# Kernel tuning notes

Hardware: AMD Instinct MI355X
Metric: run time of the kernel (lower is better)

## Reference

```python
import jax, jax.numpy as jnp
import numpy as np
from jax import lax

NUM_HEADS = 8
HEAD_DIM = 32
DIM = NUM_HEADS * HEAD_DIM  # 256
SR = 2
B, H, W = 4, 64, 64


def setup_inputs() -> dict:
    key = jax.random.key(0)
    ks = jax.random.split(key, 6)
    x = jax.random.normal(ks[0], (B, DIM, H, W), dtype=jnp.float32)
    # query: 1x1 conv without bias -> plain [out,in] matrix
    Wq = jax.random.normal(ks[1], (DIM, DIM), dtype=jnp.float32) * (1.0 / np.sqrt(DIM))
    # key/value: sr x sr conv, stride sr, no bias (OIHW)
    Wk = jax.random.normal(ks[2], (DIM, DIM, SR, SR), dtype=jnp.float32) * (1.0 / np.sqrt(DIM * SR * SR))
    Wv = jax.random.normal(ks[3], (DIM, DIM, SR, SR), dtype=jnp.float32) * (1.0 / np.sqrt(DIM * SR * SR))
    rel_h = jax.random.normal(ks[4], (1, NUM_HEADS, HEAD_DIM, 1, H // SR), dtype=jnp.float32)
    rel_w = jax.random.normal(ks[5], (1, NUM_HEADS, HEAD_DIM, W // SR, 1), dtype=jnp.float32)
    return {"x": x, "Wq": Wq, "Wk": Wk, "Wv": Wv, "rel_h": rel_h, "rel_w": rel_w}


def reference(x, Wq, Wk, Wv, rel_h, rel_w):
    b, c, h, w = x.shape
    nh, hd = NUM_HEADS, HEAD_DIM
    scale = hd ** (-0.5)
    dn = ('NCHW', 'OIHW', 'NCHW')

    # q: 1x1 conv == channel matmul; [B, C, H*W] -> [B, nh, hd, Nq]
    q = jnp.einsum('oc,bchw->bohw', Wq, x).reshape(b, nh, hd, h * w)
    # k, v: sr x sr conv, stride sr -> [B, nh, hd, Nkv]
    k = lax.conv_general_dilated(x, Wk, window_strides=(SR, SR), padding='VALID',
                                 dimension_numbers=dn).reshape(b, nh, hd, -1)
    v = lax.conv_general_dilated(x, Wv, window_strides=(SR, SR), padding='VALID',
                                 dimension_numbers=dn).reshape(b, nh, hd, -1)

    # attn scores: q^T k -> [B, nh, Nq, Nkv]
    attn = jnp.einsum('bhdn,bhdm->bhnm', q, k)
    # relative positional bias: (rel_h + rel_w) broadcast -> [nh, hd, Nkv]
    pos = (rel_h + rel_w).reshape(nh, hd, -1)
    attn = attn + jnp.einsum('bhdn,hdm->bhnm', q, pos)
    attn = jax.nn.softmax(attn * scale, axis=-1)

    # out = v @ attn^T -> [B, nh, hd, Nq] -> [B, C, H, W]
    out = jnp.einsum('bhdm,bhnm->bhdn', v, attn).reshape(b, c, h, w)
    return out
```

## Files before the change

kernel.cpp:

```cpp
#include <hip/hip_runtime.h>
#include <math.h>


typedef __bf16 bf16;
typedef __attribute__((ext_vector_type(4))) __bf16 bf16x4;
typedef __attribute__((ext_vector_type(8))) __bf16 bf16x8;
typedef __attribute__((ext_vector_type(4))) float f32x4;
typedef __attribute__((ext_vector_type(2))) __fp16 fp16x2_raw;
typedef __attribute__((ext_vector_type(4))) _Float16 f16x4;

#define MFMA16 __builtin_amdgcn_mfma_f32_16x16x32_bf16
#define MFMA16H __builtin_amdgcn_mfma_f32_16x16x16f16

#define QSCALE 0.25503486f
#define SOFTMAX_SHIFT 10.0f

__global__ void k_prep_w(const float* __restrict__ Wq, const float* __restrict__ Wk,
                         const float* __restrict__ Wv,
                         bf16* __restrict__ Wq_bf, bf16* __restrict__ Wkv_bf) {
    int tid = blockIdx.x * 256 + threadIdx.x;
    int c = tid >> 8, i = tid & 255;
    const float* Wsrc = (c < 256) ? Wk : Wv;
    int cs = c & 255;
    f32x4 w4 = ((const f32x4*)Wsrc)[cs * 256 + i];
#pragma unroll
    for (int tap = 0; tap < 4; tap++)
        Wkv_bf[c * 1024 + tap * 256 + i] = (bf16)w4[tap];
    if (tid < 16384) {
        f32x4 q4 = ((const f32x4*)Wq)[tid];
        bf16x4 o;
#pragma unroll
        for (int e = 0; e < 4; e++) o[e] = (bf16)(q4[e] * QSCALE);
        *(bf16x4*)(Wq_bf + tid * 4) = o;
    }
}

__global__ void k_xT(const float* __restrict__ x, bf16* __restrict__ xT) {
    int b = blockIdx.z, c0 = blockIdx.y * 64, n0 = blockIdx.x * 64;
    __shared__ float tile[64][65];
    int t = threadIdx.x;
    const float* xp = x + (size_t)(b * 256 + c0) * 4096 + n0;
#pragma unroll
    for (int k2 = 0; k2 < 16; k2++) {
        int flat = k2 * 256 + t;
        int row = flat >> 6, col = flat & 63;
        tile[row][col] = xp[(size_t)row * 4096 + col];
    }
    __syncthreads();
    bf16* op = xT + (size_t)(b * 4096 + n0) * 256 + c0;
#pragma unroll
    for (int k2 = 0; k2 < 16; k2++) {
        int flat = k2 * 256 + t;
        int row = flat >> 6, col = flat & 63;
        op[(size_t)row * 256 + col] = (bf16)tile[col][row];
    }
}

__launch_bounds__(256)
__global__ void k_gemm_kv(const bf16* __restrict__ xT, const bf16* __restrict__ Wkv_bf,
                          const float* __restrict__ rel_h, const float* __restrict__ rel_w,
                          bf16* __restrict__ kpos_t, _Float16* __restrict__ v_td) {
    int b = blockIdx.z;
    int bx = blockIdx.x;
    int m0 = bx * 32;
    int c0w = blockIdx.y * 64 + (threadIdx.x >> 6) * 16;
    int t = threadIdx.x, l = t & 63;
    int lr = l & 15, lg = l >> 4;
    __shared__ __align__(16) bf16 Ps[2][32 * 264];
    const bf16* xb = xT + (size_t)b * 4096 * 256;
    int srow = t >> 3;
    int scu0 = (t & 7) * 4;
    uint4 pre[4];
#define LOAD_CHUNK(tap)                                                        \
    {                                                                          \
        int dy = (tap) >> 1, dx = (tap) & 1;                                   \
        const bf16* src = xb + (size_t)((2 * bx + dy) * 64 + 2 * srow + dx) * 256; \
        _Pragma("unroll")                                                      \
        for (int j = 0; j < 4; j++)                                            \
            pre[j] = *(const uint4*)(src + (scu0 + j) * 8);                    \
    }
#define WRITE_CHUNK(buf)                                                       \
    {                                                                          \
        bf16* dst = Ps[buf] + srow * 264 + scu0 * 8;                           \
        _Pragma("unroll")                                                      \
        for (int j = 0; j < 4; j++) *(uint4*)(dst + j * 8) = pre[j];           \
    }
    LOAD_CHUNK(0)
    WRITE_CHUNK(0)
    const bf16* Gkb = Wkv_bf + (size_t)(c0w + lr) * 1024 + lg * 8;
    const bf16* Gvb = Gkb + 256 * 1024;
    f32x4 accK[2] = {}, accV[2] = {};
    for (int ch = 0; ch < 4; ch++) {
        if (ch < 3) LOAD_CHUNK(ch + 1)
        __syncthreads();
        const bf16* P = Ps[ch & 1];
#pragma unroll
        for (int kk = 0; kk < 8; kk++) {
            bf16x8 pa0 = *(const bf16x8*)(P + lr * 264 + kk * 32 + lg * 8);
            bf16x8 pa1 = *(const bf16x8*)(P + (16 + lr) * 264 + kk * 32 + lg * 8);
            bf16x8 gk = *(const bf16x8*)(Gkb + ch * 256 + kk * 32);
            bf16x8 gv = *(const bf16x8*)(Gvb + ch * 256 + kk * 32);
            accK[0] = MFMA16(pa0, gk, accK[0], 0, 0, 0);
            accK[1] = MFMA16(pa1, gk, accK[1], 0, 0, 0);
            accV[0] = MFMA16(gv, pa0, accV[0], 0, 0, 0);
            accV[1] = MFMA16(gv, pa1, accV[1], 0, 0, 0);
        }
        if (ch < 3) {
            __syncthreads();
            WRITE_CHUNK((ch + 1) & 1)
        }
    }
    {
        int cc = c0w + lr;
        float rw = rel_w[cc * 32 + bx];
#pragma unroll
        for (int i = 0; i < 2; i++)
#pragma unroll
            for (int r = 0; r < 4; r++) {
                int ml = i * 16 + lg * 4 + r;
                float val = accK[i][r] + rw + rel_h[cc * 32 + ml];
                kpos_t[((size_t)(b * 8 + (cc >> 5)) * 1024 + m0 + ml) * 32 + (cc & 31)] = (bf16)val;
            }
    }
#pragma unroll
    for (int j = 0; j < 2; j++) {
        int m = m0 + j * 16 + lr;
#pragma unroll
        for (int r = 0; r < 4; r++) {
            int cc = c0w + lg * 4 + r;
            v_td[((size_t)(b * 8 + (cc >> 5)) * 32 + (cc & 31)) * 1024 + m] = (_Float16)accV[j][r];
        }
    }
#undef LOAD_CHUNK
#undef WRITE_CHUNK
}

__launch_bounds__(256)
__global__ void k_attn(const bf16* __restrict__ xT, const bf16* __restrict__ Wq_bf,
                       const bf16* __restrict__ kpos_t, const _Float16* __restrict__ v_td,
                       float* __restrict__ out) {
    int b = blockIdx.z, h = blockIdx.y;
    int t = threadIdx.x;
    int w = t >> 6, l = t & 63;
    int n0 = blockIdx.x * 128 + w * 32;
    int lr = l & 15, lg = l >> 4;
    const size_t bh = (size_t)(b * 8 + h);
    __shared__ __align__(16) bf16 Ks[2][128 * 32];
    __shared__ __align__(16) _Float16 Vs[2][32][136];
    const bf16* Kb = kpos_t + bh * 1024 * 32;
    const _Float16* Vb = v_td + bh * 32 * 1024;
    bf16* Qs = (bf16*)Ks + w * 1280;
    {
        const bf16* Aw = Wq_bf + (size_t)(h * 32 + lr) * 256 + lg * 8;
        const bf16* Bx = xT + (size_t)(b * 4096 + n0 + lr) * 256 + lg * 8;
        f32x4 aq[2][2] = {};
#pragma unroll
        for (int kk = 0; kk < 8; kk++) {
            bf16x8 a0 = *(const bf16x8*)(Aw + kk * 32);
            bf16x8 a1 = *(const bf16x8*)(Aw + 16 * 256 + kk * 32);
            bf16x8 b0 = *(const bf16x8*)(Bx + kk * 32);
            bf16x8 b1 = *(const bf16x8*)(Bx + 16 * 256 + kk * 32);
            aq[0][0] = MFMA16(a0, b0, aq[0][0], 0, 0, 0);
            aq[0][1] = MFMA16(a0, b1, aq[0][1], 0, 0, 0);
            aq[1][0] = MFMA16(a1, b0, aq[1][0], 0, 0, 0);
            aq[1][1] = MFMA16(a1, b1, aq[1][1], 0, 0, 0);
        }
#pragma unroll
        for (int i = 0; i < 2; i++)
#pragma unroll
            for (int j = 0; j < 2; j++) {
                bf16x4 pk;
#pragma unroll
                for (int r = 0; r < 4; r++) pk[r] = (bf16)aq[i][j][r];
                *(bf16x4*)(Qs + (j * 16 + lr) * 40 + i * 16 + lg * 4) = pk;
            }
    }
    bf16x8 bq0, bq1;
    {
        bf16x4 a0 = *(const bf16x4*)(Qs + lr * 40 + lg * 8);
        bf16x4 a1 = *(const bf16x4*)(Qs + lr * 40 + lg * 8 + 4);
        bf16x4 b0 = *(const bf16x4*)(Qs + (16 + lr) * 40 + lg * 8);
        bf16x4 b1 = *(const bf16x4*)(Qs + (16 + lr) * 40 + lg * 8 + 4);
#pragma unroll
        for (int e = 0; e < 4; e++) {
            bq0[e] = a0[e]; bq0[4 + e] = a1[e];
            bq1[e] = b0[e]; bq1[4 + e] = b1[e];
        }
    }
    __syncthreads();
#define STAGE(ch, buf)                                                         \
    {                                                                          \
        const uint4* ksrc = (const uint4*)(Kb + (size_t)(ch) * 128 * 32);      \
        _Pragma("unroll")                                                      \
        for (int j = 0; j < 2; j++) {                                          \
            int u = t + j * 256;                        \
            int m = u >> 2;                                                    \
            int phys = ((m >> 1) + (u & 3)) & 3;                               \
            *(uint4*)(&Ks[buf][m * 32 + phys * 8]) = ksrc[u];                  \
        }                                                                      \
        _Pragma("unroll")                                                      \
        for (int j = 0; j < 2; j++) {                                          \
            int u = t + j * 256;                        \
            *(uint4*)(&Vs[buf][u >> 4][(u & 15) * 8]) =                        \
                *(const uint4*)(Vb + (size_t)(u >> 4) * 1024 + (ch) * 128 +    \
                                (u & 15) * 8);                                 \
        }                                                                      \
    }
    STAGE(0, 0)
    f32x4 accO[2][2] = {};
    f32x4 accS0 = {}, accS1 = {};
    const f16x4 onesv = {(_Float16)1.f, (_Float16)1.f, (_Float16)1.f, (_Float16)1.f};
    const f32x4 zs = {-SOFTMAX_SHIFT, -SOFTMAX_SHIFT, -SOFTMAX_SHIFT, -SOFTMAX_SHIFT};
    const int koff = (((lr >> 1) + lg) & 3) * 8;
    for (int ch = 0; ch < 8; ch++) {
        __syncthreads();
        if (ch < 7) STAGE(ch + 1, (ch + 1) & 1)
        const bf16* Kc = Ks[ch & 1];
#pragma unroll
        for (int tt = 0; tt < 8; tt++) {
            bf16x8 ak = *(const bf16x8*)(Kc + (tt * 16 + lr) * 32 + koff);
            f32x4 s0 = MFMA16(ak, bq0, zs, 0, 0, 0);
            f32x4 s1 = MFMA16(ak, bq1, zs, 0, 0, 0);
            f16x4 p0, p1;
            {
                fp16x2_raw c01 = __builtin_amdgcn_cvt_pkrtz(
                    __builtin_amdgcn_exp2f(s0[0]), __builtin_amdgcn_exp2f(s0[1]));
                fp16x2_raw c23 = __builtin_amdgcn_cvt_pkrtz(
                    __builtin_amdgcn_exp2f(s0[2]), __builtin_amdgcn_exp2f(s0[3]));
                p0[0] = c01[0]; p0[1] = c01[1]; p0[2] = c23[0]; p0[3] = c23[1];
                fp16x2_raw d01 = __builtin_amdgcn_cvt_pkrtz(
                    __builtin_amdgcn_exp2f(s1[0]), __builtin_amdgcn_exp2f(s1[1]));
                fp16x2_raw d23 = __builtin_amdgcn_cvt_pkrtz(
                    __builtin_amdgcn_exp2f(s1[2]), __builtin_amdgcn_exp2f(s1[3]));
                p1[0] = d01[0]; p1[1] = d01[1]; p1[2] = d23[0]; p1[3] = d23[1];
            }
            f16x4 v0 = *(const f16x4*)(&Vs[ch & 1][lr][tt * 16 + lg * 4]);
            f16x4 v1 = *(const f16x4*)(&Vs[ch & 1][16 + lr][tt * 16 + lg * 4]);
            accO[0][0] = MFMA16H(p0, v0, accO[0][0], 0, 0, 0);
            accO[0][1] = MFMA16H(p0, v1, accO[0][1], 0, 0, 0);
            accS0      = MFMA16H(p0, onesv, accS0, 0, 0, 0);
            accO[1][0] = MFMA16H(p1, v0, accO[1][0], 0, 0, 0);
            accO[1][1] = MFMA16H(p1, v1, accO[1][1], 0, 0, 0);
            accS1      = MFMA16H(p1, onesv, accS1, 0, 0, 0);
        }
    }
#undef STAGE
    float inv0[4], inv1[4];
#pragma unroll
    for (int r = 0; r < 4; r++) {
        inv0[r] = 1.0f / accS0[r];
        inv1[r] = 1.0f / accS1[r];
    }
#pragma unroll
    for (int dt = 0; dt < 2; dt++) {
        int c = h * 32 + dt * 16 + lr;
        float* op0 = out + (size_t)(b * 256 + c) * 4096 + n0 + lg * 4;
        float* op1 = op0 + 16;
        f32x4 o0, o1;
#pragma unroll
        for (int r = 0; r < 4; r++) {
            o0[r] = accO[0][dt][r] * inv0[r];
            o1[r] = accO[1][dt][r] * inv1[r];
        }
        *(f32x4*)op0 = o0;
        *(f32x4*)op1 = o1;
    }
}

extern "C" void kernel_launch(void* const* d_in, const int* in_sizes, int n_in,
                              void* d_out, int out_size, void* d_ws, size_t ws_size,
                              hipStream_t stream) {
    const float* x    = (const float*)d_in[0];
    const float* Wq   = (const float*)d_in[1];
    const float* Wk   = (const float*)d_in[2];
    const float* Wv   = (const float*)d_in[3];
    const float* relh = (const float*)d_in[4];
    const float* relw = (const float*)d_in[5];
    float* out = (float*)d_out;
    char* ws = (char*)d_ws;

    bf16*      xT     = (bf16*)(ws);
    bf16*      kposT  = (bf16*)(ws + (8u << 20));
    _Float16*  v_td   = (_Float16*)(ws + (10u << 20));
    bf16*      Wq_bf  = (bf16*)(ws + (12u << 20));
    bf16*      Wkv_bf = (bf16*)(ws + (12u << 20) + (256u << 10));

    k_prep_w <<<512,            256, 0, stream>>>(Wq, Wk, Wv, Wq_bf, Wkv_bf);
    k_xT     <<<dim3(64, 4, 4), 256, 0, stream>>>(x, xT);
    k_gemm_kv<<<dim3(32, 4, 4), 256, 0, stream>>>(xT, Wkv_bf, relh, relw, kposT, v_td);
    k_attn   <<<dim3(32, 8, 4), 256, 0, stream>>>(xT, Wq_bf, kposT, v_td, out);
}
```

Baseline: 155.3 us.

## Use 512-thread attention blocks with 16 queries per wave and register-staged prefetch

The attention kernel now runs 8 waves per block, each handling 16 queries instead of 32, so each K/V tile in shared memory is shared by twice as many waves while each wave holds fewer accumulators. K/V chunks are prefetched from global memory into registers one step ahead and written to the double-buffered shared tiles after the compute loop, leaving one barrier per chunk. The compute loop is wrapped in raised wave priority. The aim is higher occupancy and better latency hiding. In exchange there is less instruction-level parallelism per wave, and the launch bound of 8 may force register limits.

```diff
diff --git a/kernel.cpp b/kernel.cpp
--- a/kernel.cpp
+++ b/kernel.cpp
@@ -135,135 +135,113 @@
 #undef WRITE_CHUNK
 }
 
-__launch_bounds__(256)
+__launch_bounds__(512, 8)
 __global__ void k_attn(const bf16* __restrict__ xT, const bf16* __restrict__ Wq_bf,
                        const bf16* __restrict__ kpos_t, const _Float16* __restrict__ v_td,
                        float* __restrict__ out) {
     int b = blockIdx.z, h = blockIdx.y;
     int t = threadIdx.x;
     int w = t >> 6, l = t & 63;
-    int n0 = blockIdx.x * 128 + w * 32;
+    int n0 = blockIdx.x * 128 + w * 16;
     int lr = l & 15, lg = l >> 4;
     const size_t bh = (size_t)(b * 8 + h);
-    __shared__ __align__(16) bf16 Ks[2][128 * 32];
-    __shared__ __align__(16) _Float16 Vs[2][32][136];
+    __shared__ __align__(16) char smem[2 * 128 * 32 * 2 + 2 * 32 * 136 * 2];
+    bf16* KsB = (bf16*)smem;
+    _Float16* VsB = (_Float16*)(smem + 16384);
     const bf16* Kb = kpos_t + bh * 1024 * 32;
     const _Float16* Vb = v_td + bh * 32 * 1024;
-    bf16* Qs = (bf16*)Ks + w * 1280;
+    uint4 pk_r, pv_r;
+#define LOADCH(ch)                                                             \
+    {                                                                          \
+        pk_r = ((const uint4*)(Kb + (size_t)(ch) * 128 * 32))[t];              \
+        pv_r = *(const uint4*)(Vb + (size_t)(t >> 4) * 1024 + (ch) * 128 +     \
+                               (t & 15) * 8);                                  \
+    }
+#define WRITECH(buf)                                                           \
+    {                                                                          \
+        int m = t >> 2;                                                        \
+        int phys = ((m >> 1) + (t & 3)) & 3;                                   \
+        *(uint4*)(&KsB[(buf) * 4096 + m * 32 + phys * 8]) = pk_r;              \
+        *(uint4*)(&VsB[(buf) * (32 * 136) + (t >> 4) * 136 + (t & 15) * 8]) = pv_r; \
+    }
+    LOADCH(0)
+    bf16* Qs = (bf16*)smem + w * 1280;
+    bf16x8 bq0;
     {
         const bf16* Aw = Wq_bf + (size_t)(h * 32 + lr) * 256 + lg * 8;
         const bf16* Bx = xT + (size_t)(b * 4096 + n0 + lr) * 256 + lg * 8;
-        f32x4 aq[2][2] = {};
+        f32x4 aq[2] = {};
 #pragma unroll
         for (int kk = 0; kk < 8; kk++) {
             bf16x8 a0 = *(const bf16x8*)(Aw + kk * 32);
             bf16x8 a1 = *(const bf16x8*)(Aw + 16 * 256 + kk * 32);
             bf16x8 b0 = *(const bf16x8*)(Bx + kk * 32);
-            bf16x8 b1 = *(const bf16x8*)(Bx + 16 * 256 + kk * 32);
-            aq[0][0] = MFMA16(a0, b0, aq[0][0], 0, 0, 0);
-            aq[0][1] = MFMA16(a0, b1, aq[0][1], 0, 0, 0);
-            aq[1][0] = MFMA16(a1, b0, aq[1][0], 0, 0, 0);
-            aq[1][1] = MFMA16(a1, b1, aq[1][1], 0, 0, 0);
-        }
-#pragma unroll
-        for (int i = 0; i < 2; i++)
-#pragma unroll
-            for (int j = 0; j < 2; j++) {
-                bf16x4 pk;
-#pragma unroll
-                for (int r = 0; r < 4; r++) pk[r] = (bf16)aq[i][j][r];
-                *(bf16x4*)(Qs + (j * 16 + lr) * 40 + i * 16 + lg * 4) = pk;
-            }
-    }
-    bf16x8 bq0, bq1;
-    {
+            aq[0] = MFMA16(a0, b0, aq[0], 0, 0, 0);
+            aq[1] = MFMA16(a1, b0, aq[1], 0, 0, 0);
+        }
+#pragma unroll
+        for (int i = 0; i < 2; i++) {
+            bf16x4 pk;
+#pragma unroll
+            for (int r = 0; r < 4; r++) pk[r] = (bf16)aq[i][r];
+            *(bf16x4*)(Qs + lr * 40 + i * 16 + lg * 4) = pk;
+        }
         bf16x4 a0 = *(const bf16x4*)(Qs + lr * 40 + lg * 8);
         bf16x4 a1 = *(const bf16x4*)(Qs + lr * 40 + lg * 8 + 4);
-        bf16x4 b0 = *(const bf16x4*)(Qs + (16 + lr) * 40 + lg * 8);
-        bf16x4 b1 = *(const bf16x4*)(Qs + (16 + lr) * 40 + lg * 8 + 4);
-#pragma unroll
-        for (int e = 0; e < 4; e++) {
-            bq0[e] = a0[e]; bq0[4 + e] = a1[e];
-            bq1[e] = b0[e]; bq1[4 + e] = b1[e];
-        }
+#pragma unroll
+        for (int e = 0; e < 4; e++) { bq0[e] = a0[e]; bq0[4 + e] = a1[e]; }
     }
     __syncthreads();
-#define STAGE(ch, buf)                                                         \
-    {                                                                          \
-        const uint4* ksrc = (const uint4*)(Kb + (size_t)(ch) * 128 * 32);      \
-        _Pragma("unroll")                                                      \
-        for (int j = 0; j < 2; j++) {                                          \
-            int u = t + j * 256;                        \
-            int m = u >> 2;                                                    \
-            int phys = ((m >> 1) + (u & 3)) & 3;                               \
-            *(uint4*)(&Ks[buf][m * 32 + phys * 8]) = ksrc[u];                  \
-        }                                                                      \
-        _Pragma("unroll")                                                      \
-        for (int j = 0; j < 2; j++) {                                          \
-            int u = t + j * 256;                        \
-            *(uint4*)(&Vs[buf][u >> 4][(u & 15) * 8]) =                        \
-                *(const uint4*)(Vb + (size_t)(u >> 4) * 1024 + (ch) * 128 +    \
-                                (u & 15) * 8);                                 \
-        }                                                                      \
-    }
-    STAGE(0, 0)
-    f32x4 accO[2][2] = {};
-    f32x4 accS0 = {}, accS1 = {};
+    WRITECH(0)
+    LOADCH(1)
+    __syncthreads();
+    f32x4 accO[2] = {};
+    f32x4 accS = {};
     const f16x4 onesv = {(_Float16)1.f, (_Float16)1.f, (_Float16)1.f, (_Float16)1.f};
     const f32x4 zs = {-SOFTMAX_SHIFT, -SOFTMAX_SHIFT, -SOFTMAX_SHIFT, -SOFTMAX_SHIFT};
     const int koff = (((lr >> 1) + lg) & 3) * 8;
     for (int ch = 0; ch < 8; ch++) {
-        __syncthreads();
-        if (ch < 7) STAGE(ch + 1, (ch + 1) & 1)
-        const bf16* Kc = Ks[ch & 1];
+        const bf16* Kc = KsB + (ch & 1) * 4096;
+        const _Float16* Vc = VsB + (ch & 1) * (32 * 136);
+        __builtin_amdgcn_s_setprio(1);
 #pragma unroll
         for (int tt = 0; tt < 8; tt++) {
             bf16x8 ak = *(const bf16x8*)(Kc + (tt * 16 + lr) * 32 + koff);
             f32x4 s0 = MFMA16(ak, bq0, zs, 0, 0, 0);
-            f32x4 s1 = MFMA16(ak, bq1, zs, 0, 0, 0);
-            f16x4 p0, p1;
+            f16x4 p0;
             {
                 fp16x2_raw c01 = __builtin_amdgcn_cvt_pkrtz(
                     __builtin_amdgcn_exp2f(s0[0]), __builtin_amdgcn_exp2f(s0[1]));
                 fp16x2_raw c23 = __builtin_amdgcn_cvt_pkrtz(
                     __builtin_amdgcn_exp2f(s0[2]), __builtin_amdgcn_exp2f(s0[3]));
                 p0[0] = c01[0]; p0[1] = c01[1]; p0[2] = c23[0]; p0[3] = c23[1];
-                fp16x2_raw d01 = __builtin_amdgcn_cvt_pkrtz(
-                    __builtin_amdgcn_exp2f(s1[0]), __builtin_amdgcn_exp2f(s1[1]));
-                fp16x2_raw d23 = __builtin_amdgcn_cvt_pkrtz(
-                    __builtin_amdgcn_exp2f(s1[2]), __builtin_amdgcn_exp2f(s1[3]));
-                p1[0] = d01[0]; p1[1] = d01[1]; p1[2] = d23[0]; p1[3] = d23[1];
             }
-            f16x4 v0 = *(const f16x4*)(&Vs[ch & 1][lr][tt * 16 + lg * 4]);
-            f16x4 v1 = *(const f16x4*)(&Vs[ch & 1][16 + lr][tt * 16 + lg * 4]);
-            accO[0][0] = MFMA16H(p0, v0, accO[0][0], 0, 0, 0);
-            accO[0][1] = MFMA16H(p0, v1, accO[0][1], 0, 0, 0);
-            accS0      = MFMA16H(p0, onesv, accS0, 0, 0, 0);
-            accO[1][0] = MFMA16H(p1, v0, accO[1][0], 0, 0, 0);
-            accO[1][1] = MFMA16H(p1, v1, accO[1][1], 0, 0, 0);
-            accS1      = MFMA16H(p1, onesv, accS1, 0, 0, 0);
-        }
-    }
-#undef STAGE
-    float inv0[4], inv1[4];
-#pragma unroll
-    for (int r = 0; r < 4; r++) {
-        inv0[r] = 1.0f / accS0[r];
-        inv1[r] = 1.0f / accS1[r];
-    }
+            f16x4 v0 = *(const f16x4*)(Vc + lr * 136 + tt * 16 + lg * 4);
+            f16x4 v1 = *(const f16x4*)(Vc + (16 + lr) * 136 + tt * 16 + lg * 4);
+            accO[0] = MFMA16H(p0, v0, accO[0], 0, 0, 0);
+            accO[1] = MFMA16H(p0, v1, accO[1], 0, 0, 0);
+            accS    = MFMA16H(p0, onesv, accS, 0, 0, 0);
+        }
+        __builtin_amdgcn_s_setprio(0);
+        if (ch < 7) {
+            WRITECH((ch + 1) & 1)
+            if (ch < 6) LOADCH(ch + 2)
+            __syncthreads();
+        }
+    }
+#undef LOADCH
+#undef WRITECH
+    float inv[4];
+#pragma unroll
+    for (int r = 0; r < 4; r++) inv[r] = 1.0f / accS[r];
 #pragma unroll
     for (int dt = 0; dt < 2; dt++) {
         int c = h * 32 + dt * 16 + lr;
-        float* op0 = out + (size_t)(b * 256 + c) * 4096 + n0 + lg * 4;
-        float* op1 = op0 + 16;
-        f32x4 o0, o1;
-#pragma unroll
-        for (int r = 0; r < 4; r++) {
-            o0[r] = accO[0][dt][r] * inv0[r];
-            o1[r] = accO[1][dt][r] * inv1[r];
-        }
-        *(f32x4*)op0 = o0;
-        *(f32x4*)op1 = o1;
+        float* op = out + (size_t)(b * 256 + c) * 4096 + n0 + lg * 4;
+        f32x4 o;
+#pragma unroll
+        for (int r = 0; r < 4; r++) o[r] = accO[dt][r] * inv[r];
+        *(f32x4*)op = o;
     }
 }
 
@@ -288,5 +266,5 @@
     k_prep_w <<<512,            256, 0, stream>>>(Wq, Wk, Wv, Wq_bf, Wkv_bf);
     k_xT     <<<dim3(64, 4, 4), 256, 0, stream>>>(x, xT);
     k_gemm_kv<<<dim3(32, 4, 4), 256, 0, stream>>>(xT, Wkv_bf, relh, relw, kposT, v_td);
-    k_attn   <<<dim3(32, 8, 4), 256, 0, stream>>>(xT, Wq_bf, kposT, v_td, out);
-}
+    k_attn   <<<dim3(32, 8, 4), 512, 0, stream>>>(xT, Wq_bf, kposT, v_td, out);
+}
```

Result: faster. 146.5 us (-5.7%).
